# Kernel tuning notes

Hardware: AMD Instinct MI355X
Metric: run time of the kernel (lower is better)

## Reference

```python
import jax, jax.numpy as jnp
import numpy as np

PRIMES = [130003, 130021, 130027, 130043, 130051, 130057, 130069, 130073]
B, S, M, D = 4, 2048, 4, 2048   # batch, seq, hc_mult branches, hidden_size
E, H, DPH = 1024, 8, 128        # total engram embed dim, hash heads, dim per head
K, DIL = 4, 3                    # conv kernel size, dilation (= max ngram size)
EPS_GATE = 1.1920929e-07         # torch RMSNorm default eps (fp32 finfo eps)
EPS_CONV = 1e-5                  # ShortConv norm_eps


def rmsnorm(x, w, eps):
    # x: [..., D], w: broadcastable to [..., D]
    return x * jax.lax.rsqrt(jnp.mean(jnp.square(x), axis=-1, keepdims=True) + eps) * w


def setup_inputs() -> dict:
    key = jax.random.key(0)
    ks = jax.random.split(key, 8)
    total_capacity = int(sum(PRIMES))
    return {
        "hash_indices": jax.random.randint(ks[0], (B, S, H), 0, min(PRIMES)),
        "hidden_states": jax.random.normal(ks[1], (B, S, M, D), jnp.float32),
        "emb_table": jax.random.normal(ks[2], (total_capacity, DPH), jnp.float32) * 0.02,
        "w_v": jax.random.normal(ks[3], (D, E), jnp.float32) * 0.02,      # Linear(E->D) weight [out,in]
        "w_k": jax.random.normal(ks[4], (M, D, E), jnp.float32) * 0.02,   # per-branch Linear(E->D)
        "norm_h_w": jnp.ones((M, D), jnp.float32),
        "norm_k_w": jnp.ones((M, D), jnp.float32),
        "conv_norm_w": jnp.ones((M, D), jnp.float32),
        "conv_w": jax.random.normal(ks[5], (M * D, K), jnp.float32) * 0.02,  # depthwise kernel
    }


def reference(hash_indices, hidden_states, emb_table, w_v, w_k,
              norm_h_w, norm_k_w, conv_norm_w, conv_w):
    # --- multi-head hashed embedding gather (offset into concatenated tables) ---
    offsets = jnp.asarray(np.concatenate([[0], np.cumsum(PRIMES[:-1])]), jnp.int64)
    emb = emb_table[hash_indices + offsets]            # [B,S,H,DPH]
    emb = emb.reshape(B, S, E)                         # flattened engram embedding

    # --- context-aware gating ---
    value = jnp.einsum('bse,de->bsd', emb, w_v)        # [B,S,D]
    keys = jnp.einsum('bse,mde->bsmd', emb, w_k)       # [B,S,M,D]
    nk = rmsnorm(keys, norm_k_w, EPS_GATE)
    nq = rmsnorm(hidden_states, norm_h_w, EPS_GATE)
    score = jnp.sum(nk * nq, axis=-1) / jnp.sqrt(jnp.float32(D))   # [B,S,M]
    g = jnp.sqrt(jnp.maximum(jnp.abs(score), 1e-6)) * jnp.sign(score)
    gate = jax.nn.sigmoid(g)[..., None]                # [B,S,M,1]
    gated = gate * value[:, :, None, :]                # [B,S,M,D]

    # --- ShortConv: SiLU(depthwise causal Conv1d(RMSNorm(gated))) + gated ---
    xn = rmsnorm(gated, conv_norm_w, EPS_CONV)         # per-branch norm, [B,S,M,D]
    xc = xn.transpose(0, 2, 3, 1).reshape(B, M * D, S)  # [B,C,T]
    pad = (K - 1) * DIL
    xp = jnp.pad(xc, ((0, 0), (0, 0), (pad, 0)))
    conv = sum(conv_w[:, k][None, :, None]
               * jax.lax.dynamic_slice_in_dim(xp, k * DIL, S, axis=2)
               for k in range(K))                       # causal depthwise conv
    conv = jax.nn.silu(conv)
    conv = conv.reshape(B, M, D, S).transpose(0, 3, 1, 2)  # [B,S,M,D]
    short_conv_out = conv + gated

    # --- residual to transformer hidden states ---
    return hidden_states + short_conv_out
```

## Files before the change

kernel.cpp:

```cpp
#include <hip/hip_runtime.h>
#include <hip/hip_bf16.h>

#define BDIM 4
#define SDIM 2048
#define MDIM 4
#define DDIM 2048
#define EDIM 1024
#define NTOK 8192
#define NGEMM 10240
#define KDIM 1024
#define NKT 16
#define EPS_GATE 1.1920929e-07f
#define EPS_CONV 1e-5f
#define RSQRT_D 0.022097086912079608f

typedef __bf16 bf16x8 __attribute__((ext_vector_type(8)));
typedef float f32x4 __attribute__((ext_vector_type(4)));
typedef unsigned short ushort8 __attribute__((ext_vector_type(8)));

__constant__ int OFFS[8] = {0, 130003, 260024, 390051, 520094, 650145, 780202, 910271};

__device__ __forceinline__ float bf2f(unsigned short u) {
  union { unsigned int i; float f; } x; x.i = ((unsigned int)u) << 16; return x.f;
}
__device__ __forceinline__ unsigned short f2bf(float f) {
  __hip_bfloat16 h = __float2bfloat16(f);
  unsigned short u; __builtin_memcpy(&u, &h, 2); return u;
}

__global__ __launch_bounds__(256) void k_gather(const int* __restrict__ idx,
                                                const float* __restrict__ table,
                                                unsigned short* __restrict__ embb) {
  const int tok = blockIdx.x;
  const int tid = threadIdx.x;
  const int h = tid >> 5;
  const int e = (tid & 31) * 4;
  const int row = idx[tok * 8 + h] + OFFS[h];
  const float4 v = *(const float4*)(table + (size_t)row * 128 + e);
  ushort4 st;
  st.x = f2bf(v.x); st.y = f2bf(v.y); st.z = f2bf(v.z); st.w = f2bf(v.w);
  *(ushort4*)(embb + (size_t)tok * 1024 + h * 128 + e) = st;
}

__global__ __launch_bounds__(256) void k_cvtw(const float* __restrict__ wv,
                                              const float* __restrict__ wk,
                                              unsigned short* __restrict__ Wb) {
  const size_t i = ((size_t)blockIdx.x * 256 + threadIdx.x) * 4;
  const size_t NV = (size_t)DDIM * EDIM;
  float4 v;
  if (i < NV) v = *(const float4*)(wv + i);
  else        v = *(const float4*)(wk + (i - NV));
  ushort4 st;
  st.x = f2bf(v.x); st.y = f2bf(v.y); st.z = f2bf(v.z); st.w = f2bf(v.w);
  *(ushort4*)(Wb + i) = st;
}

#define GLDS(g, l) __builtin_amdgcn_global_load_lds(                        \
    (const __attribute__((address_space(1))) void*)(g),                    \
    (__attribute__((address_space(3))) void*)(l), 16, 0, 0)

#define BARR() __builtin_amdgcn_s_barrier()
#define LGK0() asm volatile("s_waitcnt lgkmcnt(0)" ::: "memory")
#define VM6()  asm volatile("s_waitcnt vmcnt(6)" ::: "memory")
#define VM0()  asm volatile("s_waitcnt vmcnt(0)" ::: "memory")
#define SB0()  __builtin_amdgcn_sched_barrier(0)

__global__ __launch_bounds__(512, 2) void k_gemm(const unsigned short* __restrict__ A,
                                                 const unsigned short* __restrict__ Bw,
                                                 unsigned short* __restrict__ Cv,
                                                 unsigned short* __restrict__ Ck)
{
  __shared__ __align__(1024) unsigned short lds[65536];
  const int tid = threadIdx.x;
  const int lane = tid & 63, wave = tid >> 6;
  const int wm = wave >> 2;
  const int wn = wave & 3;
  const int bid = blockIdx.y * gridDim.x + blockIdx.x;
  const int cpx = (gridDim.x * gridDim.y) >> 3;
  const int swz = (bid & 7) * cpx + (bid >> 3);
  const int row0 = (swz / gridDim.x) * 256;
  const int col0 = (swz % gridDim.x) * 256;
  const int lr = lane & 15;
  const int lg = lane >> 4;

  f32x4 acc[8][4] = {};
  bf16x8 aa[4][2];
  bf16x8 bb[4][2];

#define STG(src, rowbase, kt, gbase)                                           \
  { _Pragma("unroll") for (int l = 0; l < 2; ++l) {                            \
      const int cb = l * 512 + wave * 64;                                      \
      const int chunk = cb + lane;                                             \
      const int rr = chunk >> 3;                                               \
      const int cc = (chunk & 7) ^ (rr & 7);                                   \
      GLDS((src) + (size_t)((rowbase) + rr) * KDIM + (kt) * 64 + cc * 8,       \
           (char*)lds + (gbase) * 2 + cb * 16);                                \
  } }

#define LDA(gbase)                                                             \
  { _Pragma("unroll") for (int a = 0; a < 4; ++a)                              \
    _Pragma("unroll") for (int ks = 0; ks < 2; ++ks)                           \
      aa[a][ks] = *(const bf16x8*)(lds + (gbase) +                             \
          (wm * 64 + a * 16 + lr) * 64 + (((ks * 4 + lg) ^ (lr & 7)) * 8)); }

#define LDB(gbase, n0)                                                         \
  { _Pragma("unroll") for (int n = 0; n < 2; ++n)                              \
    _Pragma("unroll") for (int ks = 0; ks < 2; ++ks)                           \
      bb[(n0) + n][ks] = *(const bf16x8*)(lds + 32768 + (gbase) +              \
          (wn * 32 + n * 16 + lr) * 64 + (((ks * 4 + lg) ^ (lr & 7)) * 8)); }

#define MM(mfb, nfb)                                                           \
  { __builtin_amdgcn_s_setprio(1);                                             \
    _Pragma("unroll") for (int a = 0; a < 4; ++a)                              \
    _Pragma("unroll") for (int n = 0; n < 2; ++n)                              \
    _Pragma("unroll") for (int ks = 0; ks < 2; ++ks)                           \
      acc[(mfb) + a][(nfb) + n] = __builtin_amdgcn_mfma_f32_16x16x32_bf16(     \
          aa[a][ks], bb[(nfb) + n][ks], acc[(mfb) + a][(nfb) + n], 0, 0, 0);   \
    __builtin_amdgcn_s_setprio(0); }

  STG(A,  row0 +   0, 0, 0 * 8192);
  STG(Bw, col0 +   0, 0, 32768 + 0 * 8192);
  STG(Bw, col0 + 128, 0, 32768 + 1 * 8192);
  STG(A,  row0 + 128, 0, 1 * 8192);
  STG(A,  row0 +   0, 1, 2 * 8192);
  STG(Bw, col0 +   0, 1, 32768 + 2 * 8192);
  STG(Bw, col0 + 128, 1, 32768 + 3 * 8192);
  VM6();
  BARR(); SB0();

  for (int kt = 0; kt < NKT; ++kt) {
    const int sA = (kt & 1) * 2;
    const int sN1 = ((kt + 1) & 1) * 2;
    LDA(sA * 8192);
    LDB(sA * 8192, 0);
    if (kt + 1 < NKT) STG(A, row0 + 128, kt + 1, (sN1 + 1) * 8192);
    BARR(); LGK0(); SB0();
    MM(0, 0);
    BARR(); SB0();
    LDB((sA + 1) * 8192, 2);
    if (kt + 2 < NKT) STG(A, row0 + 0, kt + 2, sA * 8192);
    BARR(); LGK0(); SB0();
    MM(0, 2);
    BARR(); SB0();
    LDA((sA + 1) * 8192);
    if (kt + 2 < NKT) STG(Bw, col0 + 0, kt + 2, 32768 + sA * 8192);
    BARR(); LGK0(); SB0();
    MM(4, 2);
    BARR(); SB0();
    if (kt + 2 < NKT) STG(Bw, col0 + 128, kt + 2, 32768 + (sA + 1) * 8192);
    if (kt < NKT - 1) { if (kt == NKT - 2) { VM0(); } else { VM6(); } }
    BARR(); LGK0(); SB0();
    MM(4, 0);
    BARR(); SB0();
  }

  const int rb = (lane >> 4) * 4;
#pragma unroll
  for (int mf = 0; mf < 8; ++mf) {
#pragma unroll
    for (int nf = 0; nf < 4; ++nf) {
      const int grow = row0 + (mf >> 2) * 128 + wm * 64 + (mf & 3) * 16 + rb;
      const int gcol = col0 + (nf >> 1) * 128 + wn * 32 + (nf & 1) * 16 + lr;
      if (col0 < DDIM) {
        unsigned short* p = Cv + (size_t)grow * DDIM + gcol;
#pragma unroll
        for (int r = 0; r < 4; ++r) p[(size_t)r * DDIM] = f2bf(acc[mf][nf][r]);
      } else {
        unsigned short* p = Ck + (size_t)grow * 8192 + (gcol - DDIM);
#pragma unroll
        for (int r = 0; r < 4; ++r) p[(size_t)r * 8192] = f2bf(acc[mf][nf][r]);
      }
    }
  }
}

__global__ __launch_bounds__(256) void k_score(const float* __restrict__ hidden,
                                               const unsigned short* __restrict__ valueb,
                                               const unsigned short* __restrict__ keysb,
                                               const float* __restrict__ norm_h,
                                               const float* __restrict__ norm_k,
                                               float* __restrict__ gates,
                                               float* __restrict__ alphas) {
  const int tok = blockIdx.x;
  const int tid = threadIdx.x, lane = tid & 63, m = tid >> 6;
  __shared__ float smv[4];

  float pv = 0.f;
  {
    const ushort8 v8 = *(const ushort8*)(valueb + (size_t)tok * DDIM + (m * 64 + lane) * 8);
#pragma unroll
    for (int t = 0; t < 8; ++t) { const float f = bf2f(v8[t]); pv += f * f; }
  }

  const float4* hrow = (const float4*)(hidden + ((size_t)tok * 4 + m) * DDIM);
  const ushort4* krow = (const ushort4*)(keysb + (size_t)tok * 8192 + (size_t)m * DDIM);
  const float4* wkr = (const float4*)(norm_k + m * DDIM);
  const float4* whr = (const float4*)(norm_h + m * DDIM);
  float sk = 0.f, sh = 0.f, sd = 0.f;
#pragma unroll
  for (int i = 0; i < 8; ++i) {
    const int d4 = i * 64 + lane;
    const float4 h = hrow[d4];
    const float4 a = wkr[d4];
    const float4 b = whr[d4];
    const ushort4 ku = krow[d4];
    const float kx = bf2f(ku.x), ky = bf2f(ku.y), kz = bf2f(ku.z), kw = bf2f(ku.w);
    sk += kx * kx + ky * ky + kz * kz + kw * kw;
    sh += h.x * h.x + h.y * h.y + h.z * h.z + h.w * h.w;
    sd += kx * h.x * a.x * b.x + ky * h.y * a.y * b.y + kz * h.z * a.z * b.z + kw * h.w * a.w * b.w;
  }
#pragma unroll
  for (int off = 32; off > 0; off >>= 1) {
    pv += __shfl_down(pv, off);
    sk += __shfl_down(sk, off);
    sh += __shfl_down(sh, off);
    sd += __shfl_down(sd, off);
  }
  if (lane == 0) smv[m] = pv;
  __syncthreads();
  if (lane == 0) {
    const float msv = (smv[0] + smv[1] + smv[2] + smv[3]) * (1.f / 2048.f);
    const float msk = sk * (1.f / 2048.f) + EPS_GATE;
    const float msh = sh * (1.f / 2048.f) + EPS_GATE;
    const float score = sd * rsqrtf(msk) * rsqrtf(msh) * RSQRT_D;
    const float sgn = (score > 0.f) ? 1.f : ((score < 0.f) ? -1.f : 0.f);
    const float g = sqrtf(fmaxf(fabsf(score), 1e-6f)) * sgn;
    const float gate = 1.f / (1.f + expf(-g));
    gates[tok * 4 + m] = gate;
    alphas[tok * 4 + m] = gate * rsqrtf(gate * gate * msv + EPS_CONV);
  }
}

__global__ __launch_bounds__(256) void k_final(const float* __restrict__ hidden,
                                               const unsigned short* __restrict__ valueb,
                                               const float* __restrict__ gates,
                                               const float* __restrict__ alphas,
                                               const float* __restrict__ wcn,
                                               const float* __restrict__ cw,
                                               float* __restrict__ outp) {
  const long lin = (long)blockIdx.x * 256 + threadIdx.x;
  const int d4 = (int)(lin & 511);
  const int tok = (int)(lin >> 9);
  const int s = tok & (SDIM - 1);
  const int d = d4 * 4;

  float4 vj[4];
  {
    const ushort4 u = *(const ushort4*)(valueb + (size_t)tok * DDIM + d);
    vj[0] = make_float4(bf2f(u.x), bf2f(u.y), bf2f(u.z), bf2f(u.w));
  }
#pragma unroll
  for (int j = 1; j < 4; ++j) {
    if (s >= 3 * j) {
      const ushort4 u = *(const ushort4*)(valueb + (size_t)(tok - 3 * j) * DDIM + d);
      vj[j] = make_float4(bf2f(u.x), bf2f(u.y), bf2f(u.z), bf2f(u.w));
    } else vj[j] = make_float4(0.f, 0.f, 0.f, 0.f);
  }

#pragma unroll
  for (int m = 0; m < 4; ++m) {
    const float g = gates[tok * 4 + m];
    const float4 h4 = *(const float4*)(hidden + ((size_t)tok * 4 + m) * DDIM + d);
    const float4 wn = *(const float4*)(wcn + m * DDIM + d);
    float a[4];
#pragma unroll
    for (int j = 0; j < 4; ++j)
      a[j] = (s >= 3 * j) ? alphas[(tok - 3 * j) * 4 + m] : 0.f;
    float cwr[4][4];
#pragma unroll
    for (int i = 0; i < 4; ++i)
      *(float4*)cwr[i] = *(const float4*)(cw + (size_t)(m * DDIM + d + i) * 4);

    float cx = 0.f, cy = 0.f, cz = 0.f, cv = 0.f;
#pragma unroll
    for (int j = 0; j < 4; ++j) {
      const int t = 3 - j;
      const float aj = a[j];
      cx += cwr[0][t] * aj * vj[j].x;
      cy += cwr[1][t] * aj * vj[j].y;
      cz += cwr[2][t] * aj * vj[j].z;
      cv += cwr[3][t] * aj * vj[j].w;
    }
    cx *= wn.x; cy *= wn.y; cz *= wn.z; cv *= wn.w;
    cx = cx / (1.f + expf(-cx));
    cy = cy / (1.f + expf(-cy));
    cz = cz / (1.f + expf(-cz));
    cv = cv / (1.f + expf(-cv));

    float4 o;
    o.x = h4.x + g * vj[0].x + cx;
    o.y = h4.y + g * vj[0].y + cy;
    o.z = h4.z + g * vj[0].z + cz;
    o.w = h4.w + g * vj[0].w + cv;
    *(float4*)(outp + ((size_t)tok * 4 + m) * DDIM + d) = o;
  }
}

extern "C" void kernel_launch(void* const* d_in, const int* in_sizes, int n_in,
                              void* d_out, int out_size, void* d_ws, size_t ws_size,
                              hipStream_t stream) {
  const int*   hash_idx = (const int*)d_in[0];
  const float* hidden   = (const float*)d_in[1];
  const float* table    = (const float*)d_in[2];
  const float* w_v      = (const float*)d_in[3];
  const float* w_k      = (const float*)d_in[4];
  const float* norm_h   = (const float*)d_in[5];
  const float* norm_k   = (const float*)d_in[6];
  const float* wcn      = (const float*)d_in[7];
  const float* cw       = (const float*)d_in[8];
  float* outp = (float*)d_out;
  char* ws = (char*)d_ws;

  unsigned short* embb  = (unsigned short*)(ws + 0);
  unsigned short* Wb    = (unsigned short*)(ws + 16777216);
  unsigned short* value = (unsigned short*)(ws + 37748736);
  unsigned short* keysb = (unsigned short*)(ws + 71303168);
  float*          gates = (float*)(ws + 205520896);
  float*          alphas= (float*)(ws + 205651968);

  k_gather<<<NTOK, 256, 0, stream>>>(hash_idx, table, embb);
  k_cvtw<<<10240, 256, 0, stream>>>(w_v, w_k, Wb);
  dim3 gg(NGEMM / 256, NTOK / 256);
  k_gemm<<<gg, 512, 0, stream>>>(embb, Wb, value, keysb);
  k_score<<<NTOK, 256, 0, stream>>>(hidden, value, keysb, norm_h, norm_k, gates, alphas);
  k_final<<<(NTOK * DDIM / 4) / 256, 256, 0, stream>>>(hidden, value, gates, alphas, wcn, cw, outp);
}
```

Measured before the change: 465.1 us.

## Fuse gating score reductions into GEMM epilogue and tile conv over four tokens

The key GEMM epilogue now computes per-row partial sums of k², h² and the weighted k·h dot product for each 256-column panel, reading hidden states through LDS. This removes the large bf16 keys buffer write and its re-read in the score kernel. A small alpha kernel reduces the eight panel partials per token. The final kernel processes four tokens per thread so the dilated value rows are shared between them. The trade-offs are that hidden is read an extra time inside the GEMM, the key path has a heavier epilogue, and launch bounds drop to one block per SM.

Result: faster. 420.4 us (-9.6%).

```diff
diff --git a/kernel.cpp b/kernel.cpp
--- a/kernel.cpp
+++ b/kernel.cpp
@@ -10,6 +10,7 @@
 #define NGEMM 10240
 #define KDIM 1024
 #define NKT 16
+#define NPAN 8
 #define EPS_GATE 1.1920929e-07f
 #define EPS_CONV 1e-5f
 #define RSQRT_D 0.022097086912079608f
@@ -65,12 +66,18 @@
 #define VM0()  asm volatile("s_waitcnt vmcnt(0)" ::: "memory")
 #define SB0()  __builtin_amdgcn_sched_barrier(0)
 
-__global__ __launch_bounds__(512, 2) void k_gemm(const unsigned short* __restrict__ A,
+__global__ __launch_bounds__(512, 1) void k_gemm(const unsigned short* __restrict__ A,
                                                  const unsigned short* __restrict__ Bw,
+                                                 const float* __restrict__ hidden,
+                                                 const float* __restrict__ norm_h,
+                                                 const float* __restrict__ norm_k,
                                                  unsigned short* __restrict__ Cv,
-                                                 unsigned short* __restrict__ Ck)
+                                                 float* __restrict__ skP,
+                                                 float* __restrict__ sdP,
+                                                 float* __restrict__ shP)
 {
   __shared__ __align__(1024) unsigned short lds[65536];
+  __shared__ float redk[2][128][4], redd[2][128][4], redh[2][128][4];
   const int tid = threadIdx.x;
   const int lane = tid & 63, wave = tid >> 6;
   const int wm = wave >> 2;
@@ -154,78 +161,115 @@
     BARR(); SB0();
   }
 
-  const int rb = (lane >> 4) * 4;
-#pragma unroll
-  for (int mf = 0; mf < 8; ++mf) {
+  if (col0 < DDIM) {
+#pragma unroll
+    for (int mf = 0; mf < 8; ++mf) {
+#pragma unroll
+      for (int nf = 0; nf < 4; ++nf) {
+        const int grow = row0 + (mf >> 2) * 128 + wm * 64 + (mf & 3) * 16 + (lane >> 4) * 4;
+        const int gcol = col0 + (nf >> 1) * 128 + wn * 32 + (nf & 1) * 16 + lr;
+        unsigned short* p = Cv + (size_t)grow * DDIM + gcol;
+#pragma unroll
+        for (int r = 0; r < 4; ++r) p[(size_t)r * DDIM] = f2bf(acc[mf][nf][r]);
+      }
+    }
+  } else {
+    const int m = (col0 - DDIM) >> 11;
+    const int dbase = (col0 - DDIM) & (DDIM - 1);
+    const int pan = dbase >> 8;
+    float* hl = (float*)lds;
+    float wkh[4];
 #pragma unroll
     for (int nf = 0; nf < 4; ++nf) {
-      const int grow = row0 + (mf >> 2) * 128 + wm * 64 + (mf & 3) * 16 + rb;
-      const int gcol = col0 + (nf >> 1) * 128 + wn * 32 + (nf & 1) * 16 + lr;
-      if (col0 < DDIM) {
-        unsigned short* p = Cv + (size_t)grow * DDIM + gcol;
-#pragma unroll
-        for (int r = 0; r < 4; ++r) p[(size_t)r * DDIM] = f2bf(acc[mf][nf][r]);
-      } else {
-        unsigned short* p = Ck + (size_t)grow * 8192 + (gcol - DDIM);
-#pragma unroll
-        for (int r = 0; r < 4; ++r) p[(size_t)r * 8192] = f2bf(acc[mf][nf][r]);
+      const int cl = (nf >> 1) * 128 + wn * 32 + (nf & 1) * 16 + lr;
+      wkh[nf] = norm_k[m * DDIM + dbase + cl] * norm_h[m * DDIM + dbase + cl];
+    }
+#pragma unroll
+    for (int h = 0; h < 2; ++h) {
+      BARR();
+#pragma unroll
+      for (int i = 0; i < 16; ++i) {
+        const int idx = i * 512 + tid;
+        const int rl = idx >> 6;
+        const int c4 = idx & 63;
+        ((float4*)hl)[idx] = *(const float4*)(hidden +
+            ((size_t)(row0 + h * 128 + rl) * 4 + m) * DDIM + dbase + c4 * 4);
       }
-    }
-  }
-}
-
-__global__ __launch_bounds__(256) void k_score(const float* __restrict__ hidden,
-                                               const unsigned short* __restrict__ valueb,
-                                               const unsigned short* __restrict__ keysb,
-                                               const float* __restrict__ norm_h,
-                                               const float* __restrict__ norm_k,
+      BARR();
+#pragma unroll
+      for (int mf = 0; mf < 4; ++mf) {
+#pragma unroll
+        for (int r = 0; r < 4; ++r) {
+          const int rl = wm * 64 + mf * 16 + (lane >> 4) * 4 + r;
+          const int amf = h * 4 + mf;
+          float pk = 0.f, pd = 0.f, ph = 0.f;
+#pragma unroll
+          for (int nf = 0; nf < 4; ++nf) {
+            const int cl = (nf >> 1) * 128 + wn * 32 + (nf & 1) * 16 + lr;
+            const float kv = acc[amf][nf][r];
+            const float hv = hl[rl * 256 + cl];
+            pk += kv * kv; ph += hv * hv; pd += kv * hv * wkh[nf];
+          }
+#pragma unroll
+          for (int off = 1; off < 16; off <<= 1) {
+            pk += __shfl_xor(pk, off);
+            pd += __shfl_xor(pd, off);
+            ph += __shfl_xor(ph, off);
+          }
+          if (lr == 0) {
+            redk[h][rl][wn] = pk; redd[h][rl][wn] = pd; redh[h][rl][wn] = ph;
+          }
+        }
+      }
+    }
+    BARR();
+    if (tid < 256) {
+      const int h = tid >> 7, rl = tid & 127;
+      const int tok = row0 + h * 128 + rl;
+      const size_t pidx = ((size_t)tok * 4 + m) * NPAN + pan;
+      skP[pidx] = redk[h][rl][0] + redk[h][rl][1] + redk[h][rl][2] + redk[h][rl][3];
+      sdP[pidx] = redd[h][rl][0] + redd[h][rl][1] + redd[h][rl][2] + redd[h][rl][3];
+      shP[pidx] = redh[h][rl][0] + redh[h][rl][1] + redh[h][rl][2] + redh[h][rl][3];
+    }
+  }
+}
+
+__global__ __launch_bounds__(256) void k_alpha(const unsigned short* __restrict__ valueb,
+                                               const float* __restrict__ skP,
+                                               const float* __restrict__ sdP,
+                                               const float* __restrict__ shP,
                                                float* __restrict__ gates,
                                                float* __restrict__ alphas) {
   const int tok = blockIdx.x;
-  const int tid = threadIdx.x, lane = tid & 63, m = tid >> 6;
-  __shared__ float smv[4];
+  const int tid = threadIdx.x, lane = tid & 63, w = tid >> 6;
+  __shared__ float red[4];
 
   float pv = 0.f;
   {
-    const ushort8 v8 = *(const ushort8*)(valueb + (size_t)tok * DDIM + (m * 64 + lane) * 8);
+    const ushort8 v8 = *(const ushort8*)(valueb + (size_t)tok * DDIM + tid * 8);
 #pragma unroll
     for (int t = 0; t < 8; ++t) { const float f = bf2f(v8[t]); pv += f * f; }
   }
-
-  const float4* hrow = (const float4*)(hidden + ((size_t)tok * 4 + m) * DDIM);
-  const ushort4* krow = (const ushort4*)(keysb + (size_t)tok * 8192 + (size_t)m * DDIM);
-  const float4* wkr = (const float4*)(norm_k + m * DDIM);
-  const float4* whr = (const float4*)(norm_h + m * DDIM);
-  float sk = 0.f, sh = 0.f, sd = 0.f;
-#pragma unroll
-  for (int i = 0; i < 8; ++i) {
-    const int d4 = i * 64 + lane;
-    const float4 h = hrow[d4];
-    const float4 a = wkr[d4];
-    const float4 b = whr[d4];
-    const ushort4 ku = krow[d4];
-    const float kx = bf2f(ku.x), ky = bf2f(ku.y), kz = bf2f(ku.z), kw = bf2f(ku.w);
-    sk += kx * kx + ky * ky + kz * kz + kw * kw;
-    sh += h.x * h.x + h.y * h.y + h.z * h.z + h.w * h.w;
-    sd += kx * h.x * a.x * b.x + ky * h.y * a.y * b.y + kz * h.z * a.z * b.z + kw * h.w * a.w * b.w;
-  }
-#pragma unroll
-  for (int off = 32; off > 0; off >>= 1) {
-    pv += __shfl_down(pv, off);
-    sk += __shfl_down(sk, off);
-    sh += __shfl_down(sh, off);
-    sd += __shfl_down(sd, off);
-  }
-  if (lane == 0) smv[m] = pv;
+#pragma unroll
+  for (int off = 32; off > 0; off >>= 1) pv += __shfl_down(pv, off);
+  if (lane == 0) red[w] = pv;
   __syncthreads();
-  if (lane == 0) {
-    const float msv = (smv[0] + smv[1] + smv[2] + smv[3]) * (1.f / 2048.f);
+
+  if (tid < 4) {
+    const int m = tid;
+    const float msv = (red[0] + red[1] + red[2] + red[3]) * (1.f / 2048.f);
+    const size_t base = ((size_t)tok * 4 + m) * NPAN;
+    float sk = 0.f, sd = 0.f, sh = 0.f;
+#pragma unroll
+    for (int q = 0; q < NPAN; ++q) {
+      sk += skP[base + q]; sd += sdP[base + q]; sh += shP[base + q];
+    }
     const float msk = sk * (1.f / 2048.f) + EPS_GATE;
     const float msh = sh * (1.f / 2048.f) + EPS_GATE;
     const float score = sd * rsqrtf(msk) * rsqrtf(msh) * RSQRT_D;
     const float sgn = (score > 0.f) ? 1.f : ((score < 0.f) ? -1.f : 0.f);
-    const float g = sqrtf(fmaxf(fabsf(score), 1e-6f)) * sgn;
-    const float gate = 1.f / (1.f + expf(-g));
+    const float gg = sqrtf(fmaxf(fabsf(score), 1e-6f)) * sgn;
+    const float gate = 1.f / (1.f + expf(-gg));
     gates[tok * 4 + m] = gate;
     alphas[tok * 4 + m] = gate * rsqrtf(gate * gate * msv + EPS_CONV);
   }
@@ -238,61 +282,65 @@
                                                const float* __restrict__ wcn,
                                                const float* __restrict__ cw,
                                                float* __restrict__ outp) {
-  const long lin = (long)blockIdx.x * 256 + threadIdx.x;
-  const int d4 = (int)(lin & 511);
-  const int tok = (int)(lin >> 9);
-  const int s = tok & (SDIM - 1);
+  const int lin = blockIdx.x * 256 + threadIdx.x;
+  const int d4 = lin & 511;
+  const int grp = lin >> 9;
+  const int tokbase = grp * 4;
+  const int sbase = tokbase & (SDIM - 1);
   const int d = d4 * 4;
 
-  float4 vj[4];
-  {
-    const ushort4 u = *(const ushort4*)(valueb + (size_t)tok * DDIM + d);
-    vj[0] = make_float4(bf2f(u.x), bf2f(u.y), bf2f(u.z), bf2f(u.w));
-  }
-#pragma unroll
-  for (int j = 1; j < 4; ++j) {
-    if (s >= 3 * j) {
-      const ushort4 u = *(const ushort4*)(valueb + (size_t)(tok - 3 * j) * DDIM + d);
-      vj[j] = make_float4(bf2f(u.x), bf2f(u.y), bf2f(u.z), bf2f(u.w));
-    } else vj[j] = make_float4(0.f, 0.f, 0.f, 0.f);
+  float4 vrow[13];
+#pragma unroll
+  for (int ri = 0; ri < 13; ++ri) {
+    const int off = ri - 9;
+    if (sbase + off >= 0) {
+      const ushort4 u = *(const ushort4*)(valueb + (size_t)(tokbase + off) * DDIM + d);
+      vrow[ri] = make_float4(bf2f(u.x), bf2f(u.y), bf2f(u.z), bf2f(u.w));
+    } else vrow[ri] = make_float4(0.f, 0.f, 0.f, 0.f);
   }
 
 #pragma unroll
   for (int m = 0; m < 4; ++m) {
-    const float g = gates[tok * 4 + m];
-    const float4 h4 = *(const float4*)(hidden + ((size_t)tok * 4 + m) * DDIM + d);
-    const float4 wn = *(const float4*)(wcn + m * DDIM + d);
-    float a[4];
-#pragma unroll
-    for (int j = 0; j < 4; ++j)
-      a[j] = (s >= 3 * j) ? alphas[(tok - 3 * j) * 4 + m] : 0.f;
     float cwr[4][4];
 #pragma unroll
     for (int i = 0; i < 4; ++i)
       *(float4*)cwr[i] = *(const float4*)(cw + (size_t)(m * DDIM + d + i) * 4);
-
-    float cx = 0.f, cy = 0.f, cz = 0.f, cv = 0.f;
-#pragma unroll
-    for (int j = 0; j < 4; ++j) {
-      const int t = 3 - j;
-      const float aj = a[j];
-      cx += cwr[0][t] * aj * vj[j].x;
-      cy += cwr[1][t] * aj * vj[j].y;
-      cz += cwr[2][t] * aj * vj[j].z;
-      cv += cwr[3][t] * aj * vj[j].w;
-    }
-    cx *= wn.x; cy *= wn.y; cz *= wn.z; cv *= wn.w;
-    cx = cx / (1.f + expf(-cx));
-    cy = cy / (1.f + expf(-cy));
-    cz = cz / (1.f + expf(-cz));
-    cv = cv / (1.f + expf(-cv));
-
-    float4 o;
-    o.x = h4.x + g * vj[0].x + cx;
-    o.y = h4.y + g * vj[0].y + cy;
-    o.z = h4.z + g * vj[0].z + cz;
-    o.w = h4.w + g * vj[0].w + cv;
-    *(float4*)(outp + ((size_t)tok * 4 + m) * DDIM + d) = o;
+    const float4 wn = *(const float4*)(wcn + m * DDIM + d);
+    float al[13];
+#pragma unroll
+    for (int ri = 0; ri < 13; ++ri) {
+      const int off = ri - 9;
+      al[ri] = (sbase + off >= 0) ? alphas[(tokbase + off) * 4 + m] : 0.f;
+    }
+#pragma unroll
+    for (int t = 0; t < 4; ++t) {
+      const int tok = tokbase + t;
+      const float g = gates[tok * 4 + m];
+      const float4 h4 = *(const float4*)(hidden + ((size_t)tok * 4 + m) * DDIM + d);
+      float cx = 0.f, cy = 0.f, cz = 0.f, cv = 0.f;
+#pragma unroll
+      for (int j = 0; j < 4; ++j) {
+        const int ri = t + 9 - 3 * j;
+        const float aj = al[ri];
+        const int tt = 3 - j;
+        cx += cwr[0][tt] * aj * vrow[ri].x;
+        cy += cwr[1][tt] * aj * vrow[ri].y;
+        cz += cwr[2][tt] * aj * vrow[ri].z;
+        cv += cwr[3][tt] * aj * vrow[ri].w;
+      }
+      cx *= wn.x; cy *= wn.y; cz *= wn.z; cv *= wn.w;
+      cx = cx / (1.f + expf(-cx));
+      cy = cy / (1.f + expf(-cy));
+      cz = cz / (1.f + expf(-cz));
+      cv = cv / (1.f + expf(-cv));
+      const int ri0 = t + 9;
+      float4 o;
+      o.x = h4.x + g * vrow[ri0].x + cx;
+      o.y = h4.y + g * vrow[ri0].y + cy;
+      o.z = h4.z + g * vrow[ri0].z + cz;
+      o.w = h4.w + g * vrow[ri0].w + cv;
+      *(float4*)(outp + ((size_t)tok * 4 + m) * DDIM + d) = o;
+    }
   }
 }
 
@@ -314,14 +362,16 @@
   unsigned short* embb  = (unsigned short*)(ws + 0);
   unsigned short* Wb    = (unsigned short*)(ws + 16777216);
   unsigned short* value = (unsigned short*)(ws + 37748736);
-  unsigned short* keysb = (unsigned short*)(ws + 71303168);
-  float*          gates = (float*)(ws + 205520896);
-  float*          alphas= (float*)(ws + 205651968);
+  float*          skP   = (float*)(ws + 71303168);
+  float*          sdP   = (float*)(ws + 72351744);
+  float*          shP   = (float*)(ws + 73400320);
+  float*          gates = (float*)(ws + 74448896);
+  float*          alphas= (float*)(ws + 74579968);
 
   k_gather<<<NTOK, 256, 0, stream>>>(hash_idx, table, embb);
   k_cvtw<<<10240, 256, 0, stream>>>(w_v, w_k, Wb);
   dim3 gg(NGEMM / 256, NTOK / 256);
-  k_gemm<<<gg, 512, 0, stream>>>(embb, Wb, value, keysb);
-  k_score<<<NTOK, 256, 0, stream>>>(hidden, value, keysb, norm_h, norm_k, gates, alphas);
-  k_final<<<(NTOK * DDIM / 4) / 256, 256, 0, stream>>>(hidden, value, gates, alphas, wcn, cw, outp);
-}
+  k_gemm<<<gg, 512, 0, stream>>>(embb, Wb, hidden, norm_h, norm_k, value, skP, sdP, shP);
+  k_alpha<<<NTOK, 256, 0, stream>>>(value, skP, sdP, shP, gates, alphas);
+  k_final<<<(NTOK / 4) * 512 / 256, 256, 0, stream>>>(hidden, value, gates, alphas, wcn, cw, outp);
+}
```
